# Performance work log

Hardware: AMD Instinct MI355X
Metric: run time of the kernel (lower is better)

The kernel has to match this reference:

```python
import jax, jax.numpy as jnp
import numpy as np


def setup_inputs() -> dict:
    B, Lq, Lk, D, F, H = 2, 2048, 2048, 128, 128, 8
    key = jax.random.key(0)
    ks = jax.random.split(key, 8)
    X_Q = jax.random.normal(ks[0], (B, Lq, D), dtype=jnp.float32)
    X_K = jax.random.normal(ks[1], (B, Lk, D), dtype=jnp.float32)
    X_V = jax.random.normal(ks[2], (B, Lk, F), dtype=jnp.float32)
    mask = jax.random.randint(ks[3], (B, 1, Lq, Lk), 0, 2, dtype=jnp.int32)
    # xavier_normal for [H, D, D]: std = sqrt(2/(D+D))
    W_Q = jax.random.normal(ks[4], (H, D, D), dtype=jnp.float32) * np.sqrt(2.0 / (D + D))
    W_K = jax.random.normal(ks[5], (H, D, D), dtype=jnp.float32) * np.sqrt(2.0 / (D + D))
    W_V = jax.random.normal(ks[6], (H, F, F), dtype=jnp.float32) * np.sqrt(2.0 / (F + F))
    O = jax.random.normal(ks[7], (F * H, F), dtype=jnp.float32) * np.sqrt(2.0 / (F * H + F))
    return {"X_Q": X_Q, "X_K": X_K, "X_V": X_V, "mask": mask,
            "W_Q": W_Q, "W_K": W_K, "W_V": W_V, "O": O}


def reference(X_Q, X_K, X_V, mask, W_Q, W_K, W_V, O):
    B, Lq, D = X_Q.shape
    H = W_Q.shape[0]
    F = W_V.shape[1]
    # torch.einsum with repeated in-operand index ('hdd') takes the diagonal
    dq = jnp.diagonal(W_Q, axis1=1, axis2=2)  # [H, D]
    dk = jnp.diagonal(W_K, axis1=1, axis2=2)  # [H, D]
    dv = jnp.diagonal(W_V, axis1=1, axis2=2)  # [H, F]
    g = dq * dk                               # fused per-head QK diagonal scale [H, D]
    scale = 1.0 / jnp.sqrt(jnp.asarray(D, dtype=X_Q.dtype))
    scores = jnp.einsum('bqd,hd,bkd->bhqk', X_Q, g, X_K) * scale  # [B,H,Lq,Lk]
    scores = jnp.where(mask == 0, jnp.asarray(-jnp.inf, scores.dtype), scores)
    A = jax.nn.softmax(scores, axis=-1)
    # O_h = A @ (diag(dv_h) scaled V)
    Oh = jnp.einsum('bhqk,hf,bkf->bhqf', A, dv, X_V)  # [B,H,Lq,F]
    Oh = Oh.transpose(0, 2, 1, 3).reshape(B, Lq, H * F)
    return jnp.einsum('bqx,xf->bqf', Oh, O)
```

## Files before the change

### kernel.cpp

```cpp
#include <hip/hip_runtime.h>

typedef __bf16 bf16;
typedef __bf16 bf16x4 __attribute__((ext_vector_type(4)));
typedef __bf16 bf16x8 __attribute__((ext_vector_type(8)));
typedef float f32x4 __attribute__((ext_vector_type(4)));
typedef short s16x4 __attribute__((ext_vector_type(4)));
typedef unsigned int u32;
typedef unsigned long long u64;

#define B_ 2
#define H_ 8
#define L_ 2048
#define D_ 128
#define F_ 128
#define QT 64
#define KT 64
#define NKT (L_ / KT)

#define WS_KB 0u
#define WS_VT (1u << 20)
#define WS_MB (2u << 20)

#define SMEM_BYTES 66048
#define LWS_OFF 65536
#define POX_STRIDE 132
#define SOH_OFF 36864
#define SOH_STRIDE 136
#define SO2_STRIDE 136

__device__ __forceinline__ void dma16(const void* g, void* l) {
    __builtin_amdgcn_global_load_lds(
        (const __attribute__((address_space(1))) u32*)g,
        (__attribute__((address_space(3))) u32*)l, 16, 0, 0);
}

__device__ __forceinline__ f32x4 mfma32(bf16x8 a, bf16x8 b, f32x4 c) {
    return __builtin_amdgcn_mfma_f32_16x16x32_bf16(a, b, c, 0, 0, 0);
}

__device__ __forceinline__ f32x4 mfma16(bf16x4 a, bf16x4 b, f32x4 c) {
#if __has_builtin(__builtin_amdgcn_mfma_f32_16x16x16_bf16)
    return __builtin_amdgcn_mfma_f32_16x16x16_bf16(a, b, c, 0, 0, 0);
#else
    s16x4 as = __builtin_bit_cast(s16x4, a);
    s16x4 bs = __builtin_bit_cast(s16x4, b);
    return __builtin_amdgcn_mfma_f32_16x16x16bf16_1k(as, bs, c, 0, 0, 0);
#endif
}

__device__ __forceinline__ float fexp2(float x) {
#if __has_builtin(__builtin_amdgcn_exp2f)
    return __builtin_amdgcn_exp2f(x);
#else
    float r;
    asm("v_exp_f32 %0, %1" : "=v"(r) : "v"(x));
    return r;
#endif
}

__device__ __forceinline__ u64 spread4(u64 v) {
    v = (v | (v << 24)) & 0x000000ff000000ffULL;
    v = (v | (v << 12)) & 0x000f000f000f000fULL;
    v = (v | (v << 6))  & 0x0303030303030303ULL;
    v = (v | (v << 3))  & 0x1111111111111111ULL;
    return v;
}

__global__ __launch_bounds__(256)
void prep_one(const float* __restrict__ XK, const float* __restrict__ XV,
              const int* __restrict__ mask, bf16* __restrict__ Kb,
              bf16* __restrict__ Vtb, u64* __restrict__ bits,
              float* __restrict__ out)
{
    const int bid = blockIdx.x;
    const int tid = threadIdx.x;
    if (bid < 2048) {
        const int lane = tid & 63;
        const int wv   = bid * 4 + (tid >> 6);
        const int4* m4 = (const int4*)mask;
        #pragma unroll
        for (int t = 0; t < 4; ++t) {
            int W = wv + t * 8192;
            int4 v = m4[(size_t)W * 64 + lane];
            int nib = (v.x != 0 ? 1 : 0) | (v.y != 0 ? 2 : 0)
                    | (v.z != 0 ? 4 : 0) | (v.w != 0 ? 8 : 0);
            u64 b0 = __ballot(nib & 1);
            u64 b1 = __ballot(nib & 2);
            u64 b2 = __ballot(nib & 4);
            u64 b3 = __ballot(nib & 8);
            if (lane < 4) {
                int sh = lane * 16;
                u64 w = spread4((b0 >> sh) & 0xFFFFull)
                      | (spread4((b1 >> sh) & 0xFFFFull) << 1)
                      | (spread4((b2 >> sh) & 0xFFFFull) << 2)
                      | (spread4((b3 >> sh) & 0xFFFFull) << 3);
                bits[(size_t)W * 4 + lane] = w;
            }
        }
    } else if (bid < 2304) {
        int gid = (bid - 2048) * 256 + tid;
        int row = gid >> 4;
        int j   = gid & 15;
        const float* src = XK + (size_t)row * 128 + j * 8;
        float4 v0 = *(const float4*)src;
        float4 v1 = *(const float4*)(src + 4);
        bf16x8 w;
        w[0] = (bf16)v0.x; w[1] = (bf16)v0.y; w[2] = (bf16)v0.z; w[3] = (bf16)v0.w;
        w[4] = (bf16)v1.x; w[5] = (bf16)v1.y; w[6] = (bf16)v1.z; w[7] = (bf16)v1.w;
        int jp = j ^ (row & 15);
        *(bf16x8*)(Kb + (size_t)row * 128 + jp * 8) = w;
    } else if (bid < 2560) {
        int idx  = bid - 2304;
        int tile = idx >> 2;
        int fq   = idx & 3;
        int f    = fq * 32 + (tid & 31);
        int j    = tid >> 5;
        int bb   = tile >> 5, kt = tile & 31;
        const float* src = XV + ((size_t)(bb * L_ + kt * 64 + j * 8)) * F_ + f;
        bf16x4 w0, w1;
        #pragma unroll
        for (int jj = 0; jj < 4; ++jj) {
            w0[jj] = (bf16)src[(size_t)jj * F_];
            w1[jj] = (bf16)src[(size_t)(4 + jj) * F_];
        }
        bf16* outp = Vtb + (size_t)tile * 8192 + f * 64;
        *(bf16x4*)(outp + (((2 * j) ^ (f & 15)) * 4)) = w0;
        *(bf16x4*)(outp + (((2 * j + 1) ^ (f & 15)) * 4)) = w1;
    } else {
        float4* o4 = (float4*)out;
        int idx = (bid - 2560) * 256 + tid;
        float4 z; z.x = 0.f; z.y = 0.f; z.z = 0.f; z.w = 0.f;
        #pragma unroll
        for (int t = 0; t < 4; ++t) o4[idx + t * 32768] = z;
    }
}

__global__ __launch_bounds__(512)
__attribute__((amdgpu_waves_per_eu(4, 4)))
void attn_fused_kernel(const float* __restrict__ XQ, const bf16* __restrict__ Kb,
                       const bf16* __restrict__ Vtb, const u64* __restrict__ bits,
                       const float* __restrict__ WQ, const float* __restrict__ WK,
                       const float* __restrict__ WV, const float* __restrict__ Om,
                       float* __restrict__ out)
{
    __shared__ __align__(16) char smem[SMEM_BYTES];
    __shared__ __align__(16) float g_s[128];

    bf16* sK0 = (bf16*)smem;
    bf16* sK1 = (bf16*)(smem + 16384);
    bf16* sV0 = (bf16*)(smem + 32768);
    bf16* sV1 = (bf16*)(smem + 49152);
    float* lws = (float*)(smem + LWS_OFF);
    float* pOx = (float*)smem;
    bf16* sOh  = (bf16*)(smem + SOH_OFF);
    bf16* sO2t = (bf16*)smem;

    const int tid  = threadIdx.x;
    const int wave = tid >> 6;
    const int lane = tid & 63;
    const int c    = lane & 15;
    const int quad = lane >> 4;
    const int qt = blockIdx.x, h = blockIdx.y, b = blockIdx.z;
    const int q0 = qt * QT;

    const int kh   = wave >> 2;
    const int msel = wave & 3;
    const int fv  = tid & 127;
    const int grp = tid >> 7;

    if (tid < 128) {
        float wq = WQ[(h * D_ + tid) * D_ + tid];
        float wk = WK[(h * D_ + tid) * D_ + tid];
        g_s[tid] = wq * wk * 0.08838834764831845f * 1.4426950408889634f;
    }
    __syncthreads();

    const char* gKbase = (const char*)Kb + (size_t)(b * L_) * 256;
    const char* gVbase = (const char*)Vtb + (size_t)(b * NKT) * 16384;

    #pragma unroll
    for (int i = 0; i < 2; ++i) dma16(gKbase + i * 8192 + tid * 16, (char*)sK0 + i * 8192 + tid * 16);
    #pragma unroll
    for (int i = 0; i < 2; ++i) dma16(gVbase + i * 8192 + tid * 16, (char*)sV0 + i * 8192 + tid * 16);

    const u64* mrow = bits + (size_t)(b * L_ + q0 + msel * 16 + c) * NKT;
    u64 mbc = mrow[0];

    int koff[2][4];
    #pragma unroll
    for (int kti = 0; kti < 2; ++kti)
        #pragma unroll
        for (int kc = 0; kc < 4; ++kc)
            koff[kti][kc] = ((((kh * 2 + kti) * 16 + c) * 128) + (((kc * 4 + quad) ^ c) * 8)) * 2;
    int voff[8][2];
    #pragma unroll
    for (int fi = 0; fi < 8; ++fi)
        #pragma unroll
        for (int kti = 0; kti < 2; ++kti) {
            int g = kh * 8 + kti * 4 + quad;
            voff[fi][kti] = (((fi * 16 + c) * 64) + ((g ^ c) * 4)) * 2;
        }

    bf16x8 qfrag[4];
    {
        const float* qrow = XQ + (size_t)(b * L_ + q0 + msel * 16 + c) * D_;
        #pragma unroll
        for (int kc = 0; kc < 4; ++kc) {
            int d0 = kc * 32 + quad * 8;
            float4 v0 = *(const float4*)(qrow + d0);
            float4 v1 = *(const float4*)(qrow + d0 + 4);
            float4 g0 = *(const float4*)(g_s + d0);
            float4 g1 = *(const float4*)(g_s + d0 + 4);
            bf16x8 w;
            w[0] = (bf16)(v0.x * g0.x); w[1] = (bf16)(v0.y * g0.y);
            w[2] = (bf16)(v0.z * g0.z); w[3] = (bf16)(v0.w * g0.w);
            w[4] = (bf16)(v1.x * g1.x); w[5] = (bf16)(v1.y * g1.y);
            w[6] = (bf16)(v1.z * g1.z); w[7] = (bf16)(v1.w * g1.w);
            qfrag[kc] = w;
        }
    }

    f32x4 oacc[8];
    #pragma unroll
    for (int fi = 0; fi < 8; ++fi)
        #pragma unroll
        for (int r = 0; r < 4; ++r) oacc[fi][r] = 0.f;
    float lsum = 0.f;

    #pragma unroll 2
    for (int kt = 0; kt < NKT; ++kt) {
        const char* sK  = (kt & 1) ? (char*)sK1 : (char*)sK0;
        const char* sV  = (kt & 1) ? (char*)sV1 : (char*)sV0;
        bf16* sKn = (kt & 1) ? sK0 : sK1;
        bf16* sVn = (kt & 1) ? sV0 : sV1;

        asm volatile("s_barrier" ::: "memory");

        u64 mb = mbc;

        if (kt + 1 < NKT) {
            const char* gk = gKbase + (size_t)(kt + 1) * 16384;
            const char* gv = gVbase + (size_t)(kt + 1) * 16384;
            #pragma unroll
            for (int i = 0; i < 2; ++i) dma16(gk + i * 8192 + tid * 16, (char*)sKn + i * 8192 + tid * 16);
            #pragma unroll
            for (int i = 0; i < 2; ++i) dma16(gv + i * 8192 + tid * 16, (char*)sVn + i * 8192 + tid * 16);
            mbc = mrow[kt + 1];
            asm volatile("s_waitcnt vmcnt(5)" ::: "memory");
        } else {
            asm volatile("s_waitcnt vmcnt(0)" ::: "memory");
        }
        asm volatile("s_barrier" ::: "memory");

        __builtin_amdgcn_s_setprio(1);

        f32x4 tacc[2];
        #pragma unroll
        for (int kti = 0; kti < 2; ++kti)
            #pragma unroll
            for (int r = 0; r < 4; ++r) tacc[kti][r] = 0.f;

        #pragma unroll
        for (int kti = 0; kti < 2; ++kti) {
            #pragma unroll
            for (int kc = 0; kc < 4; ++kc) {
                bf16x8 kfrag = *(const bf16x8*)(sK + koff[kti][kc]);
                tacc[kti] = mfma32(kfrag, qfrag[kc], tacc[kti]);
            }
        }

        bf16x4 pfrag[2];
        #pragma unroll
        for (int kti = 0; kti < 2; ++kti) {
            #pragma unroll
            for (int r = 0; r < 4; ++r) {
                float p = ((mb >> (kh * 32 + kti * 16 + quad * 4 + r)) & 1ull)
                          ? fexp2(tacc[kti][r]) : 0.f;
                lsum += p;
                pfrag[kti][r] = (bf16)p;
            }
        }

        #pragma unroll
        for (int fi = 0; fi < 8; ++fi) {
            #pragma unroll
            for (int kti = 0; kti < 2; ++kti) {
                bf16x4 vfrag = *(const bf16x4*)(sV + voff[fi][kti]);
                oacc[fi] = mfma16(pfrag[kti], vfrag, oacc[fi]);
            }
        }

        __builtin_amdgcn_s_setprio(0);
    }

    {
        float v = lsum;
        v += __shfl_xor(v, 16); v += __shfl_xor(v, 32);
        if (lane < 16) lws[wave * 16 + lane] = v;
    }
    if (tid < 128)
        g_s[tid] = WV[(h * F_ + tid) * F_ + tid];
    __syncthreads();

    if (kh == 1) {
        #pragma unroll
        for (int fi = 0; fi < 8; ++fi)
            #pragma unroll
            for (int r = 0; r < 4; ++r)
                pOx[(msel * 16 + quad * 4 + r) * POX_STRIDE + fi * 16 + c] = oacc[fi][r];
    }
    __syncthreads();

    if (kh == 0) {
        float linv[4];
        #pragma unroll
        for (int r = 0; r < 4; ++r) {
            int m16 = quad * 4 + r;
            linv[r] = 1.0f / (lws[msel * 16 + m16] + lws[(4 + msel) * 16 + m16]);
        }
        #pragma unroll
        for (int fi = 0; fi < 8; ++fi)
            #pragma unroll
            for (int r = 0; r < 4; ++r) {
                int row = msel * 16 + quad * 4 + r;
                float v = (oacc[fi][r] + pOx[row * POX_STRIDE + fi * 16 + c]) * linv[r];
                sOh[row * SOH_STRIDE + fi * 16 + c] = (bf16)v;
            }
    }
    __syncthreads();

    #pragma unroll
    for (int i = 0; i < 8; ++i) {
        int fp4 = grp * 32 + i * 4;
        bf16x4 w;
        #pragma unroll
        for (int j = 0; j < 4; ++j) {
            int x = fp4 + j;
            w[j] = (bf16)(Om[(h * F_ + x) * F_ + fv] * g_s[x]);
        }
        *(bf16x4*)(sO2t + fv * SO2_STRIDE + fp4) = w;
    }
    __syncthreads();

    const int pm = wave & 3;
    const int pf = wave >> 2;
    bf16x8 afr[4];
    const bf16* ohrow = sOh + (pm * 16 + c) * SOH_STRIDE;
    #pragma unroll
    for (int kc = 0; kc < 4; ++kc)
        afr[kc] = *(const bf16x8*)(ohrow + kc * 32 + quad * 8);

    #pragma unroll
    for (int nt = 0; nt < 4; ++nt) {
        f32x4 pacc;
        #pragma unroll
        for (int r = 0; r < 4; ++r) pacc[r] = 0.f;
        const bf16* orow = sO2t + ((pf * 4 + nt) * 16 + c) * SO2_STRIDE;
        #pragma unroll
        for (int kc = 0; kc < 4; ++kc) {
            bf16x8 bfrag = *(const bf16x8*)(orow + kc * 32 + quad * 8);
            pacc = mfma32(afr[kc], bfrag, pacc);
        }
        #pragma unroll
        for (int r = 0; r < 4; ++r) {
            int qg = q0 + pm * 16 + quad * 4 + r;
            atomicAdd(out + ((size_t)(b * L_ + qg) * F_ + (pf * 4 + nt) * 16 + c), pacc[r]);
        }
    }
}

extern "C" void kernel_launch(void* const* d_in, const int* in_sizes, int n_in,
                              void* d_out, int out_size, void* d_ws, size_t ws_size,
                              hipStream_t stream) {
    const float* XQ   = (const float*)d_in[0];
    const float* XK   = (const float*)d_in[1];
    const float* XV   = (const float*)d_in[2];
    const int*   mask = (const int*)d_in[3];
    const float* WQ   = (const float*)d_in[4];
    const float* WK   = (const float*)d_in[5];
    const float* WV   = (const float*)d_in[6];
    const float* Om   = (const float*)d_in[7];
    float* out = (float*)d_out;

    char* ws = (char*)d_ws;
    bf16* Kb   = (bf16*)(ws + WS_KB);
    bf16* Vtb  = (bf16*)(ws + WS_VT);
    u64*  bits = (u64*)(ws + WS_MB);

    prep_one<<<2688, 256, 0, stream>>>(XK, XV, mask, Kb, Vtb, bits, out);

    dim3 grid(L_ / QT, H_, B_);
    attn_fused_kernel<<<grid, 512, 0, stream>>>(XQ, Kb, Vtb, bits, WQ, WK, WV, Om, out);
}
```

Before: 153.7 us.

## Read V fragments directly from global memory instead of staging through LDS

V tiles are no longer double-buffered in shared memory. Each wave now loads its V fragments straight from global memory, using a new unswizzled transposed V layout written by the prep kernel. The cross-wave reduction of partial outputs is split into two halves so it fits in less shared memory, and the occupancy hint is raised to 6 waves per EU. This cuts LDS use and DMA traffic to allow more resident blocks, but the PV MFMAs now wait on global/L2 load latency inside the inner loop.

```diff
diff --git a/kernel.cpp b/kernel.cpp
--- a/kernel.cpp
+++ b/kernel.cpp
@@ -21,10 +21,11 @@
 #define WS_VT (1u << 20)
 #define WS_MB (2u << 20)
 
-#define SMEM_BYTES 66048
-#define LWS_OFF 65536
-#define POX_STRIDE 132
-#define SOH_OFF 36864
+#define SMEM_BYTES 52736
+#define LWS_OFF 52224
+#define POX_OFF 17408
+#define POX_STRIDE 68
+#define SOH_OFF 34816
 #define SOH_STRIDE 136
 #define SO2_STRIDE 136
 
@@ -123,9 +124,9 @@
             w0[jj] = (bf16)src[(size_t)jj * F_];
             w1[jj] = (bf16)src[(size_t)(4 + jj) * F_];
         }
-        bf16* outp = Vtb + (size_t)tile * 8192 + f * 64;
-        *(bf16x4*)(outp + (((2 * j) ^ (f & 15)) * 4)) = w0;
-        *(bf16x4*)(outp + (((2 * j + 1) ^ (f & 15)) * 4)) = w1;
+        bf16* outp = Vtb + (size_t)tile * 8192;
+        *(bf16x4*)(outp + (2 * j) * 512 + f * 4) = w0;
+        *(bf16x4*)(outp + (2 * j + 1) * 512 + f * 4) = w1;
     } else {
         float4* o4 = (float4*)out;
         int idx = (bid - 2560) * 256 + tid;
@@ -136,7 +137,7 @@
 }
 
 __global__ __launch_bounds__(512)
-__attribute__((amdgpu_waves_per_eu(4, 4)))
+__attribute__((amdgpu_waves_per_eu(6)))
 void attn_fused_kernel(const float* __restrict__ XQ, const bf16* __restrict__ Kb,
                        const bf16* __restrict__ Vtb, const u64* __restrict__ bits,
                        const float* __restrict__ WQ, const float* __restrict__ WK,
@@ -148,10 +149,8 @@
 
     bf16* sK0 = (bf16*)smem;
     bf16* sK1 = (bf16*)(smem + 16384);
-    bf16* sV0 = (bf16*)(smem + 32768);
-    bf16* sV1 = (bf16*)(smem + 49152);
     float* lws = (float*)(smem + LWS_OFF);
-    float* pOx = (float*)smem;
+    float* pOx = (float*)(smem + POX_OFF);
     bf16* sOh  = (bf16*)(smem + SOH_OFF);
     bf16* sO2t = (bf16*)smem;
 
@@ -180,8 +179,6 @@
 
     #pragma unroll
     for (int i = 0; i < 2; ++i) dma16(gKbase + i * 8192 + tid * 16, (char*)sK0 + i * 8192 + tid * 16);
-    #pragma unroll
-    for (int i = 0; i < 2; ++i) dma16(gVbase + i * 8192 + tid * 16, (char*)sV0 + i * 8192 + tid * 16);
 
     const u64* mrow = bits + (size_t)(b * L_ + q0 + msel * 16 + c) * NKT;
     u64 mbc = mrow[0];
@@ -198,7 +195,7 @@
         #pragma unroll
         for (int kti = 0; kti < 2; ++kti) {
             int g = kh * 8 + kti * 4 + quad;
-            voff[fi][kti] = (((fi * 16 + c) * 64) + ((g ^ c) * 4)) * 2;
+            voff[fi][kti] = g * 1024 + (fi * 16 + c) * 8;
         }
 
     bf16x8 qfrag[4];
@@ -230,9 +227,8 @@
     #pragma unroll 2
     for (int kt = 0; kt < NKT; ++kt) {
         const char* sK  = (kt & 1) ? (char*)sK1 : (char*)sK0;
-        const char* sV  = (kt & 1) ? (char*)sV1 : (char*)sV0;
         bf16* sKn = (kt & 1) ? sK0 : sK1;
-        bf16* sVn = (kt & 1) ? sV0 : sV1;
+        const char* gVt = gVbase + (size_t)kt * 16384;
 
         asm volatile("s_barrier" ::: "memory");
 
@@ -240,13 +236,10 @@
 
         if (kt + 1 < NKT) {
             const char* gk = gKbase + (size_t)(kt + 1) * 16384;
-            const char* gv = gVbase + (size_t)(kt + 1) * 16384;
             #pragma unroll
             for (int i = 0; i < 2; ++i) dma16(gk + i * 8192 + tid * 16, (char*)sKn + i * 8192 + tid * 16);
-            #pragma unroll
-            for (int i = 0; i < 2; ++i) dma16(gv + i * 8192 + tid * 16, (char*)sVn + i * 8192 + tid * 16);
             mbc = mrow[kt + 1];
-            asm volatile("s_waitcnt vmcnt(5)" ::: "memory");
+            asm volatile("s_waitcnt vmcnt(3)" ::: "memory");
         } else {
             asm volatile("s_waitcnt vmcnt(0)" ::: "memory");
         }
@@ -285,7 +278,7 @@
         for (int fi = 0; fi < 8; ++fi) {
             #pragma unroll
             for (int kti = 0; kti < 2; ++kti) {
-                bf16x4 vfrag = *(const bf16x4*)(sV + voff[fi][kti]);
+                bf16x4 vfrag = *(const bf16x4*)(gVt + voff[fi][kti]);
                 oacc[fi] = mfma16(pfrag[kti], vfrag, oacc[fi]);
             }
         }
@@ -302,32 +295,37 @@
         g_s[tid] = WV[(h * F_ + tid) * F_ + tid];
     __syncthreads();
 
-    if (kh == 1) {
-        #pragma unroll
-        for (int fi = 0; fi < 8; ++fi)
-            #pragma unroll
-            for (int r = 0; r < 4; ++r)
-                pOx[(msel * 16 + quad * 4 + r) * POX_STRIDE + fi * 16 + c] = oacc[fi][r];
-    }
-    __syncthreads();
-
+    float linv[4];
     if (kh == 0) {
-        float linv[4];
         #pragma unroll
         for (int r = 0; r < 4; ++r) {
             int m16 = quad * 4 + r;
             linv[r] = 1.0f / (lws[msel * 16 + m16] + lws[(4 + msel) * 16 + m16]);
         }
-        #pragma unroll
-        for (int fi = 0; fi < 8; ++fi)
-            #pragma unroll
-            for (int r = 0; r < 4; ++r) {
-                int row = msel * 16 + quad * 4 + r;
-                float v = (oacc[fi][r] + pOx[row * POX_STRIDE + fi * 16 + c]) * linv[r];
-                sOh[row * SOH_STRIDE + fi * 16 + c] = (bf16)v;
-            }
-    }
-    __syncthreads();
+    }
+
+    #pragma unroll
+    for (int r2 = 0; r2 < 2; ++r2) {
+        if (kh == 1) {
+            #pragma unroll
+            for (int fl = 0; fl < 4; ++fl)
+                #pragma unroll
+                for (int r = 0; r < 4; ++r)
+                    pOx[(msel * 16 + quad * 4 + r) * POX_STRIDE + fl * 16 + c] = oacc[r2 * 4 + fl][r];
+        }
+        __syncthreads();
+        if (kh == 0) {
+            #pragma unroll
+            for (int fl = 0; fl < 4; ++fl)
+                #pragma unroll
+                for (int r = 0; r < 4; ++r) {
+                    int row = msel * 16 + quad * 4 + r;
+                    float v = (oacc[r2 * 4 + fl][r] + pOx[row * POX_STRIDE + fl * 16 + c]) * linv[r];
+                    sOh[row * SOH_STRIDE + (r2 * 4 + fl) * 16 + c] = (bf16)v;
+                }
+        }
+        __syncthreads();
+    }
 
     #pragma unroll
     for (int i = 0; i < 8; ++i) {
```

After: 433.1 us. +181.8%, slower.

## Permute K rows so PV product uses single 16x16x32 MFMA per tile

Applied to the files above, without the earlier changes.

Rows of K within each 64-row tile are permuted during the bf16 prep pass so each lane's score outputs line up with a contiguous 8-element k slice. The P·V product can then use one 16x16x32 bf16 MFMA per output fragment instead of two 16x16x16 MFMAs. The mask bit indexing and V LDS offsets are adjusted to match. This halves the MFMA instruction count in the PV step, at the cost of packing two 4-wide V loads into an 8-wide operand.

```diff
diff --git a/kernel.cpp b/kernel.cpp
--- a/kernel.cpp
+++ b/kernel.cpp
@@ -36,16 +36,6 @@
 
 __device__ __forceinline__ f32x4 mfma32(bf16x8 a, bf16x8 b, f32x4 c) {
     return __builtin_amdgcn_mfma_f32_16x16x32_bf16(a, b, c, 0, 0, 0);
-}
-
-__device__ __forceinline__ f32x4 mfma16(bf16x4 a, bf16x4 b, f32x4 c) {
-#if __has_builtin(__builtin_amdgcn_mfma_f32_16x16x16_bf16)
-    return __builtin_amdgcn_mfma_f32_16x16x16_bf16(a, b, c, 0, 0, 0);
-#else
-    s16x4 as = __builtin_bit_cast(s16x4, a);
-    s16x4 bs = __builtin_bit_cast(s16x4, b);
-    return __builtin_amdgcn_mfma_f32_16x16x16bf16_1k(as, bs, c, 0, 0, 0);
-#endif
 }
 
 __device__ __forceinline__ float fexp2(float x) {
@@ -107,8 +97,11 @@
         bf16x8 w;
         w[0] = (bf16)v0.x; w[1] = (bf16)v0.y; w[2] = (bf16)v0.z; w[3] = (bf16)v0.w;
         w[4] = (bf16)v1.x; w[5] = (bf16)v1.y; w[6] = (bf16)v1.z; w[7] = (bf16)v1.w;
-        int jp = j ^ (row & 15);
-        *(bf16x8*)(Kb + (size_t)row * 128 + jp * 8) = w;
+        int k63  = row & 63;
+        int p63  = (k63 & 32) | ((k63 & 4) << 2) | ((k63 & 24) >> 1) | (k63 & 3);
+        int prow = (row & ~63) | p63;
+        int jp = j ^ (prow & 15);
+        *(bf16x8*)(Kb + (size_t)prow * 128 + jp * 8) = w;
     } else if (bid < 2560) {
         int idx  = bid - 2304;
         int tile = idx >> 2;
@@ -185,6 +178,7 @@
 
     const u64* mrow = bits + (size_t)(b * L_ + q0 + msel * 16 + c) * NKT;
     u64 mbc = mrow[0];
+    const int mshift = kh * 32 + quad * 8;
 
     int koff[2][4];
     #pragma unroll
@@ -196,9 +190,9 @@
     #pragma unroll
     for (int fi = 0; fi < 8; ++fi)
         #pragma unroll
-        for (int kti = 0; kti < 2; ++kti) {
-            int g = kh * 8 + kti * 4 + quad;
-            voff[fi][kti] = (((fi * 16 + c) * 64) + ((g ^ c) * 4)) * 2;
+        for (int half = 0; half < 2; ++half) {
+            int g = kh * 8 + quad * 2 + half;
+            voff[fi][half] = (((fi * 16 + c) * 64) + ((g ^ c) * 4)) * 2;
         }
 
     bf16x8 qfrag[4];
@@ -269,25 +263,26 @@
             }
         }
 
-        bf16x4 pfrag[2];
+        bf16x8 apack;
         #pragma unroll
         for (int kti = 0; kti < 2; ++kti) {
             #pragma unroll
             for (int r = 0; r < 4; ++r) {
-                float p = ((mb >> (kh * 32 + kti * 16 + quad * 4 + r)) & 1ull)
+                float p = ((mb >> (mshift + kti * 4 + r)) & 1ull)
                           ? fexp2(tacc[kti][r]) : 0.f;
                 lsum += p;
-                pfrag[kti][r] = (bf16)p;
+                apack[kti * 4 + r] = (bf16)p;
             }
         }
 
         #pragma unroll
         for (int fi = 0; fi < 8; ++fi) {
-            #pragma unroll
-            for (int kti = 0; kti < 2; ++kti) {
-                bf16x4 vfrag = *(const bf16x4*)(sV + voff[fi][kti]);
-                oacc[fi] = mfma16(pfrag[kti], vfrag, oacc[fi]);
-            }
+            bf16x4 vlo = *(const bf16x4*)(sV + voff[fi][0]);
+            bf16x4 vhi = *(const bf16x4*)(sV + voff[fi][1]);
+            bf16x8 v8;
+            #pragma unroll
+            for (int r = 0; r < 4; ++r) { v8[r] = vlo[r]; v8[4 + r] = vhi[r]; }
+            oacc[fi] = mfma32(apack, v8, oacc[fi]);
         }
 
         __builtin_amdgcn_s_setprio(0);
```

Result: no change. 150.9 us (-1.8%).
